# Optimization experiments

Hardware: AMD Instinct MI355X
Metric: run time of the kernel (lower is better)

The kernel has to match this reference:

```python
import jax, jax.numpy as jnp
import numpy as np

B, S, D, H = 2, 2048, 1024, 16
DK = D // H
FF_HIDDEN = 2048  # FeedForward default hidden_dim (fixed, not 4*D)


def setup_inputs() -> dict:
    key = jax.random.key(0)
    ks = jax.random.split(key, 16)
    s = 0.02
    inp = {
        "query": jax.random.normal(ks[0], (B, S, D), jnp.float32),
        "key": jax.random.normal(ks[1], (B, S, D), jnp.float32),
        "value": jax.random.normal(ks[2], (B, S, D), jnp.float32),
        "Wq": jax.random.normal(ks[3], (D, D), jnp.float32) * s,
        "bq": jnp.zeros((D,), jnp.float32),
        "Wk": jax.random.normal(ks[4], (D, D), jnp.float32) * s,
        "bk": jnp.zeros((D,), jnp.float32),
        "Wv": jax.random.normal(ks[5], (D, D), jnp.float32) * s,
        "bv": jnp.zeros((D,), jnp.float32),
        "ln_g": jnp.ones((D,), jnp.float32),
        "ln_b": jnp.zeros((D,), jnp.float32),
        "W1": jax.random.normal(ks[6], (D, FF_HIDDEN), jnp.float32) * s,
        "b1": jnp.zeros((FF_HIDDEN,), jnp.float32),
        "W2": jax.random.normal(ks[7], (FF_HIDDEN, D), jnp.float32) * s,
        "b2": jnp.zeros((D,), jnp.float32),
    }
    return inp


def reference(query, key, value, Wq, bq, Wk, bk, Wv, bv, ln_g, ln_b, W1, b1, W2, b2):
    # QKV projections
    q = query @ Wq + bq  # [B,S,D]
    k = key @ Wk + bk
    v = value @ Wv + bv
    # split heads -> [B,H,S,DK]
    q = q.reshape(B, S, H, DK).transpose(0, 2, 1, 3)
    k = k.reshape(B, S, H, DK).transpose(0, 2, 1, 3)
    v = v.reshape(B, S, H, DK).transpose(0, 2, 1, 3)
    # naive attention: full [B,H,S,S] scores (faithful to source)
    scores = jnp.einsum("bhqd,bhkd->bhqk", q, k) / jnp.sqrt(jnp.float32(DK))
    probs = jax.nn.softmax(scores, axis=-1)  # dropout = identity (eval)
    attn = jnp.einsum("bhqk,bhkd->bhqd", probs, v)
    attn = attn.transpose(0, 2, 1, 3).reshape(B, S, D)
    # LayerNorm
    mu = attn.mean(axis=-1, keepdims=True)
    var = attn.var(axis=-1, keepdims=True)
    ffi = (attn - mu) / jnp.sqrt(var + 1e-5) * ln_g + ln_b
    # FeedForward (dropout = identity in eval)
    h = jax.nn.relu(ffi @ W1 + b1)
    ff = h @ W2 + b2
    return ffi + ff
```

## Files before the change

kernel.cpp:

```cpp
#include <hip/hip_runtime.h>
#include <hip/hip_bf16.h>


#define S_LEN 2048
#define DMODEL 1024
#define NROWS 4096
#define QSCALE (0.125f * 1.4426950408889634f)

typedef __attribute__((ext_vector_type(8))) short short8_t;
typedef __attribute__((ext_vector_type(4))) float f32x4;

__device__ __forceinline__ unsigned short f2bf(float f){
  union { float f; unsigned int u; } a; a.f = f;
  unsigned int r = a.u + 0x7fffu + ((a.u >> 16) & 1u);
  return (unsigned short)(r >> 16);
}
__device__ __forceinline__ unsigned int pack2(float lo, float hi){
  return (unsigned int)f2bf(lo) | ((unsigned int)f2bf(hi) << 16);
}
__device__ __forceinline__ unsigned int cvtpk(float lo, float hi){
  unsigned int r;
  asm("v_cvt_pk_bf16_f32 %0, %1, %2" : "=v"(r) : "v"(lo), "v"(hi));
  return r;
}
__device__ __forceinline__ void gload_lds16(const void* g, void* l){
  __builtin_amdgcn_global_load_lds((const __attribute__((address_space(1))) unsigned int*)g,
                                   (__attribute__((address_space(3))) unsigned int*)l, 16, 0, 0);
}

__global__ __launch_bounds__(256) void cast3_kernel(const float* __restrict__ q,
    const float* __restrict__ k, const float* __restrict__ v, unsigned short* __restrict__ out){
  const float* src = blockIdx.y == 0 ? q : (blockIdx.y == 1 ? k : v);
  size_t i = (size_t)(blockIdx.x * 256 + threadIdx.x) * 8;
  float4 a = *(const float4*)(src + i);
  float4 b = *(const float4*)(src + i + 4);
  uint4 u; u.x = pack2(a.x,a.y); u.y = pack2(a.z,a.w); u.z = pack2(b.x,b.y); u.w = pack2(b.z,b.w);
  *(uint4*)(out + (size_t)blockIdx.y*4194304 + i) = u;
}

__device__ __forceinline__ void tc_body(const float* __restrict__ in,
    unsigned short* __restrict__ out, int R, int C, int bx, int by){
  __shared__ __align__(16) unsigned short tile[64*76];
  int c0 = bx * 64, r0 = by * 64;
  int t = threadIdx.x;
#pragma unroll
  for (int i = 0; i < 4; i++){
    int slot = i*256 + t;
    int r = slot >> 4, c4 = slot & 15;
    float4 v = *(const float4*)(in + (size_t)(r0 + r)*C + c0 + c4*4);
    ushort4 u; u.x = f2bf(v.x); u.y = f2bf(v.y); u.z = f2bf(v.z); u.w = f2bf(v.w);
    *(ushort4*)&tile[r*76 + c4*4] = u;
  }
  __syncthreads();
#pragma unroll
  for (int i = 0; i < 4; i++){
    int slot = i*256 + t;
    int oc = slot >> 4, seg = slot & 15;
    ushort4 u;
    u.x = tile[(seg*4+0)*76 + oc];
    u.y = tile[(seg*4+1)*76 + oc];
    u.z = tile[(seg*4+2)*76 + oc];
    u.w = tile[(seg*4+3)*76 + oc];
    *(ushort4*)(out + (size_t)(c0 + oc)*R + r0 + seg*4) = u;
  }
}
__global__ __launch_bounds__(256) void transpose_cast_f32(const float* __restrict__ in,
    unsigned short* __restrict__ out, int R, int C){
  tc_body(in, out, R, C, blockIdx.x, blockIdx.y);
}
__global__ __launch_bounds__(256) void transpose_cast_w3(const float* __restrict__ w0,
    const float* __restrict__ w1, const float* __restrict__ w2, unsigned short* __restrict__ out){
  const float* in = blockIdx.z == 0 ? w0 : (blockIdx.z == 1 ? w1 : w2);
  tc_body(in, out + (size_t)blockIdx.z*1048576, 1024, 1024, blockIdx.x, blockIdx.y);
}

__global__ __launch_bounds__(256) void transpose_bf16(const unsigned short* __restrict__ in,
    unsigned short* __restrict__ out, int R, int C, int inStride){
  __shared__ __align__(16) unsigned short tile[64*76];
  int c0 = blockIdx.x * 64, r0 = blockIdx.y * 64;
  int t = threadIdx.x;
#pragma unroll
  for (int i = 0; i < 2; i++){
    int slot = i*256 + t;
    int r = slot >> 3, c8 = slot & 7;
    uint4 v = *(const uint4*)(in + (size_t)(r0 + r)*inStride + c0 + c8*8);
    uint2 lo; lo.x = v.x; lo.y = v.y;
    uint2 hi; hi.x = v.z; hi.y = v.w;
    *(uint2*)&tile[r*76 + c8*8]     = lo;
    *(uint2*)&tile[r*76 + c8*8 + 4] = hi;
  }
  __syncthreads();
#pragma unroll
  for (int i = 0; i < 4; i++){
    int slot = i*256 + t;
    int oc = slot >> 4, seg = slot & 15;
    ushort4 u;
    u.x = tile[(seg*4+0)*76 + oc];
    u.y = tile[(seg*4+1)*76 + oc];
    u.z = tile[(seg*4+2)*76 + oc];
    u.w = tile[(seg*4+3)*76 + oc];
    *(ushort4*)(out + (size_t)(c0 + oc)*R + r0 + seg*4) = u;
  }
}

__global__ __launch_bounds__(256) void concat_bias(const float* __restrict__ a,
    const float* __restrict__ b, const float* __restrict__ c, float* __restrict__ o){
  int i = blockIdx.x*256 + threadIdx.x;
  o[i] = i < 1024 ? a[i] : (i < 2048 ? b[i-1024] : c[i-2048]);
}

template<bool OBF16, bool RELU, bool RESID, int NF>
__global__ __launch_bounds__(256, 2) void gemm_bt(
    const unsigned short* __restrict__ A, const unsigned short* __restrict__ Bt,
    const float* __restrict__ bias, float scale, int scale_ncols, size_t aSel,
    unsigned short* __restrict__ Ob, float* __restrict__ Of,
    const float* __restrict__ resid, int M, int N, int K)
{
  __shared__ __align__(16) unsigned short As[128*32];
  __shared__ __align__(16) unsigned short Bs[128*32];
  int tid = threadIdx.x; int lane = tid & 63; int wave = tid >> 6;
  int wr = wave >> 1, wc = wave & 1;
  int m0 = blockIdx.y * 128, n0 = blockIdx.x * (32*NF);
  int qr = lane & 15, g = lane >> 4;
  f32x4 acc[4][NF];
#pragma unroll
  for (int i = 0; i < 4; i++)
#pragma unroll
    for (int j = 0; j < NF; j++) acc[i][j] = (f32x4){0.f,0.f,0.f,0.f};

  const unsigned short* Ag = A + (size_t)(n0 >> 10)*aSel + (size_t)(m0 + (tid >> 2))*K + (tid & 3)*8;
  const unsigned short* Bg = Bt + (size_t)(n0 + (tid >> 2))*K + (tid & 3)*8;
  char* Adst = (char*)As + wave*1024;
  char* Bdst = (char*)Bs + wave*1024;

  for (int k0 = 0; k0 < K; k0 += 32){
    gload_lds16(Ag + k0,                  Adst);
    gload_lds16(Ag + (size_t)64*K + k0,   Adst + 4096);
    gload_lds16(Bg + k0,                  Bdst);
    if constexpr (NF == 4)
      gload_lds16(Bg + (size_t)64*K + k0, Bdst + 4096);
    __syncthreads();
    short8_t af[4], bfv[NF];
#pragma unroll
    for (int mi = 0; mi < 4; mi++)  af[mi]  = *(const short8_t*)&As[(wr*64 + mi*16 + qr)*32 + g*8];
#pragma unroll
    for (int ni = 0; ni < NF; ni++) bfv[ni] = *(const short8_t*)&Bs[(wc*16*NF + ni*16 + qr)*32 + g*8];
#pragma unroll
    for (int mi = 0; mi < 4; mi++)
#pragma unroll
      for (int ni = 0; ni < NF; ni++)
        acc[mi][ni] = __builtin_amdgcn_mfma_f32_16x16x32_bf16(af[mi], bfv[ni], acc[mi][ni], 0, 0, 0);
    __syncthreads();
  }
#pragma unroll
  for (int ni = 0; ni < NF; ni++){
    int col = n0 + wc*16*NF + ni*16 + qr;
    float bs = bias[col];
    float sc = (col < scale_ncols) ? scale : 1.f;
#pragma unroll
    for (int mi = 0; mi < 4; mi++){
#pragma unroll
      for (int r = 0; r < 4; r++){
        int row = m0 + wr*64 + mi*16 + g*4 + r;
        float v = (acc[mi][ni][r] + bs) * sc;
        if constexpr (RELU) v = fmaxf(v, 0.f);
        if constexpr (RESID) v += resid[(size_t)row*N + col];
        if constexpr (OBF16) Ob[(size_t)row*N + col] = f2bf(v);
        else                 Of[(size_t)row*N + col] = v;
      }
    }
  }
}

__global__ __launch_bounds__(256, 4) void flash_attn(
    const unsigned short* __restrict__ qkv,
    const unsigned short* __restrict__ vT,
    float* __restrict__ attn)
{
  __shared__ __align__(16) char smem[40960];
  int tid = threadIdx.x, lane = tid & 63, wave = tid >> 6;
  int bid = blockIdx.x;
  int orig = (bid & 7) * 128 + (bid >> 3);
  int bh = orig >> 5, qb = orig & 31;
  int b = bh >> 4, h = bh & 15;
  int q0 = qb * 64 + wave * 16;
  int qr = lane & 15, g = lane >> 4;

  const unsigned short* qptr = qkv + (size_t)(b*S_LEN + q0 + qr)*3072 + h*64 + g*8;
  short8_t qf0 = *(const short8_t*)qptr;
  short8_t qf1 = *(const short8_t*)(qptr + 32);

  const f32x4 z4 = {0.f,0.f,0.f,0.f};
  f32x4 oacc[4];
#pragma unroll
  for (int tv = 0; tv < 4; tv++) oacc[tv] = z4;
  float lsum = 0.f;

  int lrow = lane >> 3, lslot = lane & 7;
  int sw = (lslot ^ lrow) * 8;
  const unsigned short* kg = qkv + 1024 + (size_t)(b*S_LEN + wave*8 + lrow)*3072 + h*64 + sw;
  const unsigned short* vg = vT + (size_t)(h*64 + wave*8 + lrow)*4096 + b*S_LEN + sw;

  int rx = qr & 7;
  int koff0 = qr*128 + ((g ^ rx) * 16);
  int koff1 = koff0 ^ 64;

  char* Pb = smem + 32768 + wave*2048;
  int gh = g >> 1;
  int pw0 = qr*128 + 8*(g & 1);
  int pr0 = qr*128;

  {
    char* kb_ = smem + wave*1024;
    char* vb_ = smem + 16384 + wave*1024;
    gload_lds16(kg,                       kb_);
    gload_lds16(kg + (size_t)32*3072,     kb_ + 4096);
    gload_lds16(vg,                       vb_);
    gload_lds16(vg + (size_t)32*4096,     vb_ + 4096);
  }

  int cur = 0;
  for (int it = 0; it < S_LEN/64; ++it){
    if (it + 1 < S_LEN/64){
      int kv1 = (it + 1) * 64;
      char* kb_ = smem + (cur^1)*8192 + wave*1024;
      char* vb_ = smem + 16384 + (cur^1)*8192 + wave*1024;
      gload_lds16(kg + (size_t)kv1*3072,        kb_);
      gload_lds16(kg + (size_t)(kv1+32)*3072,   kb_ + 4096);
      gload_lds16(vg + kv1,                     vb_);
      gload_lds16(vg + (size_t)32*4096 + kv1,   vb_ + 4096);
      asm volatile("s_waitcnt vmcnt(4)" ::: "memory");
    } else {
      asm volatile("s_waitcnt vmcnt(0)" ::: "memory");
    }
    __builtin_amdgcn_s_barrier();
    asm volatile("" ::: "memory");

    const char* kb = smem + cur*8192;
    const char* vb = smem + 16384 + cur*8192;

    f32x4 st[4];
    __builtin_amdgcn_s_setprio(1);
#pragma unroll
    for (int t = 0; t < 4; t++){
      short8_t kf0 = *(const short8_t*)(kb + koff0 + t*2048);
      short8_t kf1 = *(const short8_t*)(kb + koff1 + t*2048);
      st[t] = __builtin_amdgcn_mfma_f32_16x16x32_bf16(kf0, qf0, z4, 0, 0, 0);
      st[t] = __builtin_amdgcn_mfma_f32_16x16x32_bf16(kf1, qf1, st[t], 0, 0, 0);
    }
    __builtin_amdgcn_s_setprio(0);

    float ps0 = 0.f, ps1 = 0.f;
#pragma unroll
    for (int t = 0; t < 4; t++){
      float p0 = exp2f(st[t][0]);
      float p1 = exp2f(st[t][1]);
      float p2 = exp2f(st[t][2]);
      float p3 = exp2f(st[t][3]);
      uint2 wv; wv.x = cvtpk(p0, p1); wv.y = cvtpk(p2, p3);
      *(uint2*)(Pb + pw0 + (((2*t + gh) ^ rx) << 4)) = wv;
      ps0 += p0 + p1;
      ps1 += p2 + p3;
    }
    lsum += ps0 + ps1;

    short8_t pf0 = *(const short8_t*)(Pb + pr0 + (((0 + g) ^ rx) << 4));
    short8_t pf1 = *(const short8_t*)(Pb + pr0 + (((4 + g) ^ rx) << 4));

    __builtin_amdgcn_s_setprio(1);
#pragma unroll
    for (int tv = 0; tv < 4; tv++){
      short8_t vf0 = *(const short8_t*)(vb + koff0 + tv*2048);
      short8_t vf1 = *(const short8_t*)(vb + koff1 + tv*2048);
      oacc[tv] = __builtin_amdgcn_mfma_f32_16x16x32_bf16(vf0, pf0, oacc[tv], 0, 0, 0);
      oacc[tv] = __builtin_amdgcn_mfma_f32_16x16x32_bf16(vf1, pf1, oacc[tv], 0, 0, 0);
    }
    __builtin_amdgcn_s_setprio(0);

    asm volatile("s_waitcnt lgkmcnt(0)" ::: "memory");
    __builtin_amdgcn_s_barrier();
    asm volatile("" ::: "memory");
    cur ^= 1;
  }
  lsum += __shfl_xor(lsum, 16, 64);
  lsum += __shfl_xor(lsum, 32, 64);
  float inv = 1.f / lsum;

  __syncthreads();
  float* ot = (float*)(smem + wave*4160);
#pragma unroll
  for (int tv = 0; tv < 4; tv++)
#pragma unroll
    for (int r = 0; r < 4; r++)
      ot[qr*65 + tv*16 + g*4 + r] = oacc[tv][r] * inv;
  __syncthreads();
  int row = lane >> 2, seg = lane & 3;
  const float* src = ot + row*65 + seg*16;
  float* dst = attn + (size_t)(b*S_LEN + qb*64 + wave*16 + row)*DMODEL + h*64 + seg*16;
#pragma unroll
  for (int i = 0; i < 4; i++){
    float4 v; v.x = src[i*4]; v.y = src[i*4+1]; v.z = src[i*4+2]; v.w = src[i*4+3];
    *(float4*)(dst + i*4) = v;
  }
}

__global__ __launch_bounds__(256) void layernorm_kernel(const float* __restrict__ x,
    const float* __restrict__ gw, const float* __restrict__ bw,
    float* __restrict__ y, unsigned short* __restrict__ yb)
{
  int row = blockIdx.x, t = threadIdx.x;
  float4 v = *(const float4*)(x + (size_t)row*DMODEL + t*4);
  float s = (v.x + v.y) + (v.z + v.w);
  float q = (v.x*v.x + v.y*v.y) + (v.z*v.z + v.w*v.w);
#pragma unroll
  for (int off = 1; off < 64; off <<= 1){
    s += __shfl_xor(s, off, 64);
    q += __shfl_xor(q, off, 64);
  }
  __shared__ float red[8];
  if ((t & 63) == 0){ red[(t >> 6)*2] = s; red[(t >> 6)*2 + 1] = q; }
  __syncthreads();
  s = red[0] + red[2] + red[4] + red[6];
  q = red[1] + red[3] + red[5] + red[7];
  float mu = s * (1.f/DMODEL);
  float var = q * (1.f/DMODEL) - mu*mu;
  float rstd = rsqrtf(var + 1e-5f);
  float4 gg = *(const float4*)(gw + t*4);
  float4 bb = *(const float4*)(bw + t*4);
  float4 o;
  o.x = (v.x - mu)*rstd*gg.x + bb.x;
  o.y = (v.y - mu)*rstd*gg.y + bb.y;
  o.z = (v.z - mu)*rstd*gg.z + bb.z;
  o.w = (v.w - mu)*rstd*gg.w + bb.w;
  *(float4*)(y + (size_t)row*DMODEL + t*4) = o;
  uint2 u; u.x = pack2(o.x, o.y); u.y = pack2(o.z, o.w);
  *(uint2*)(yb + (size_t)row*DMODEL + t*4) = u;
}

extern "C" void kernel_launch(void* const* d_in, const int* in_sizes, int n_in,
                              void* d_out, int out_size, void* d_ws, size_t ws_size,
                              hipStream_t stream)
{
  const float* query = (const float*)d_in[0];
  const float* key_  = (const float*)d_in[1];
  const float* value = (const float*)d_in[2];
  const float* Wq = (const float*)d_in[3];
  const float* bq = (const float*)d_in[4];
  const float* Wk = (const float*)d_in[5];
  const float* bk = (const float*)d_in[6];
  const float* Wv = (const float*)d_in[7];
  const float* bv = (const float*)d_in[8];
  const float* ln_g = (const float*)d_in[9];
  const float* ln_b = (const float*)d_in[10];
  const float* W1 = (const float*)d_in[11];
  const float* b1 = (const float*)d_in[12];
  const float* W2 = (const float*)d_in[13];
  const float* b2 = (const float*)d_in[14];

  char* ws = (char*)d_ws;
  unsigned short* qx     = (unsigned short*)(ws + 0);
  unsigned short* WqkvT  = (unsigned short*)(ws + 25165824);
  unsigned short* W1T    = (unsigned short*)(ws + 31457280);
  unsigned short* W2T    = (unsigned short*)(ws + 35651584);
  unsigned short* qkvbuf = (unsigned short*)(ws + 39845888);
  unsigned short* vTb    = (unsigned short*)(ws + 65011712);
  float*          attnf  = (float*)(ws + 73400320);
  unsigned short* hbuf   = (unsigned short*)(ws + 73400320);
  float*          biascat= (float*)(ws + 73400320 + 8388608);
  float*          ffif   = (float*)(ws + 90177536);
  unsigned short* ffib   = (unsigned short*)(ws + 106954752);

  cast3_kernel<<<dim3(2048,3), 256, 0, stream>>>(query, key_, value, qx);
  transpose_cast_w3<<<dim3(16,16,3), 256, 0, stream>>>(Wq, Wk, Wv, WqkvT);
  transpose_cast_f32<<<dim3(32,16), 256, 0, stream>>>(W1, W1T, 1024, 2048);
  transpose_cast_f32<<<dim3(16,32), 256, 0, stream>>>(W2, W2T, 2048, 1024);
  concat_bias<<<12, 256, 0, stream>>>(bq, bk, bv, biascat);

  gemm_bt<true,false,false,4><<<dim3(24,32), 256, 0, stream>>>(
      qx, WqkvT, biascat, QSCALE, 1024, (size_t)4194304, qkvbuf, nullptr, nullptr, 4096, 3072, 1024);
  transpose_bf16<<<dim3(16,64), 256, 0, stream>>>(qkvbuf + 2048, vTb, 4096, 1024, 3072);
  flash_attn<<<1024, 256, 0, stream>>>(qkvbuf, vTb, attnf);
  layernorm_kernel<<<4096, 256, 0, stream>>>(attnf, ln_g, ln_b, ffif, ffib);
  gemm_bt<true,true,false,4><<<dim3(16,32), 256, 0, stream>>>(
      ffib, W1T, b1, 1.f, 0, (size_t)0, hbuf, nullptr, nullptr, 4096, 2048, 1024);
  gemm_bt<false,false,true,2><<<dim3(16,32), 256, 0, stream>>>(
      hbuf, W2T, b2, 1.f, 0, (size_t)0, nullptr, (float*)d_out, ffif, 4096, 1024, 2048);
}
```

Measured before the change: 206.5 us.

## Double-buffer GEMM LDS tiles with K=64 steps and XOR-swizzled layout

Rewrites the bf16 GEMM main loop to double-buffer the A and B shared-memory tiles and prefetch the next K-chunk while computing the current one. It uses manual vmcnt waits and raw barriers in place of __syncthreads. The K step doubles to 64, halving the number of barriers per tile, and an XOR swizzle on the LDS column index is meant to avoid bank conflicts. The cost is double the LDS footprint, which may reduce occupancy, plus hand-counted waitcnt values that must match the number of issued loads.

```diff
diff --git a/kernel.cpp b/kernel.cpp
--- a/kernel.cpp
+++ b/kernel.cpp
@@ -116,9 +116,11 @@
     unsigned short* __restrict__ Ob, float* __restrict__ Of,
     const float* __restrict__ resid, int M, int N, int K)
 {
-  __shared__ __align__(16) unsigned short As[128*32];
-  __shared__ __align__(16) unsigned short Bs[128*32];
-  int tid = threadIdx.x; int lane = tid & 63; int wave = tid >> 6;
+  __shared__ __align__(16) unsigned short As[2*128*64];
+  __shared__ __align__(16) unsigned short Bs[2*32*NF*64];
+  char* AsB = (char*)As;
+  char* BsB = (char*)Bs;
+  int tid = threadIdx.x, lane = tid & 63, wave = tid >> 6;
   int wr = wave >> 1, wc = wave & 1;
   int m0 = blockIdx.y * 128, n0 = blockIdx.x * (32*NF);
   int qr = lane & 15, g = lane >> 4;
@@ -128,29 +130,67 @@
 #pragma unroll
     for (int j = 0; j < NF; j++) acc[i][j] = (f32x4){0.f,0.f,0.f,0.f};
 
-  const unsigned short* Ag = A + (size_t)(n0 >> 10)*aSel + (size_t)(m0 + (tid >> 2))*K + (tid & 3)*8;
-  const unsigned short* Bg = Bt + (size_t)(n0 + (tid >> 2))*K + (tid & 3)*8;
-  char* Adst = (char*)As + wave*1024;
-  char* Bdst = (char*)Bs + wave*1024;
-
-  for (int k0 = 0; k0 < K; k0 += 32){
-    gload_lds16(Ag + k0,                  Adst);
-    gload_lds16(Ag + (size_t)64*K + k0,   Adst + 4096);
-    gload_lds16(Bg + k0,                  Bdst);
-    if constexpr (NF == 4)
-      gload_lds16(Bg + (size_t)64*K + k0, Bdst + 4096);
-    __syncthreads();
-    short8_t af[4], bfv[NF];
-#pragma unroll
-    for (int mi = 0; mi < 4; mi++)  af[mi]  = *(const short8_t*)&As[(wr*64 + mi*16 + qr)*32 + g*8];
-#pragma unroll
-    for (int ni = 0; ni < NF; ni++) bfv[ni] = *(const short8_t*)&Bs[(wc*16*NF + ni*16 + qr)*32 + g*8];
-#pragma unroll
-    for (int mi = 0; mi < 4; mi++)
-#pragma unroll
-      for (int ni = 0; ni < NF; ni++)
-        acc[mi][ni] = __builtin_amdgcn_mfma_f32_16x16x32_bf16(af[mi], bfv[ni], acc[mi][ni], 0, 0, 0);
-    __syncthreads();
+  int lr = lane >> 3, ls = lane & 7;
+  int scol = (ls ^ lr) * 8;
+  const unsigned short* Ag = A + (size_t)(n0 >> 10)*aSel + (size_t)(m0 + wave*32 + lr)*K + scol;
+  const unsigned short* Bg = Bt + (size_t)(n0 + wave*8*NF + lr)*K + scol;
+
+  int rx = qr & 7;
+  int aoff = (wr*64 + qr)*128 + ((g ^ rx) << 4);
+  int boff = (wc*16*NF + qr)*128 + ((g ^ rx) << 4);
+
+  int NT = K >> 6;
+#pragma unroll
+  for (int i = 0; i < 4; i++)
+    gload_lds16(Ag + (size_t)i*8*K, AsB + wave*4096 + i*1024);
+#pragma unroll
+  for (int i = 0; i < NF; i++)
+    gload_lds16(Bg + (size_t)i*8*K, BsB + wave*NF*1024 + i*1024);
+
+  for (int it = 0; it < NT; ++it){
+    int cur = it & 1;
+    if (it + 1 < NT){
+      int k1 = (it + 1) << 6;
+      char* ad = AsB + (cur^1)*16384 + wave*4096;
+      char* bd = BsB + (cur^1)*NF*4096 + wave*NF*1024;
+#pragma unroll
+      for (int i = 0; i < 4; i++)
+        gload_lds16(Ag + (size_t)i*8*K + k1, ad + i*1024);
+#pragma unroll
+      for (int i = 0; i < NF; i++)
+        gload_lds16(Bg + (size_t)i*8*K + k1, bd + i*1024);
+      if constexpr (NF == 4) asm volatile("s_waitcnt vmcnt(8)" ::: "memory");
+      else                   asm volatile("s_waitcnt vmcnt(6)" ::: "memory");
+    } else {
+      asm volatile("s_waitcnt vmcnt(0)" ::: "memory");
+    }
+    __builtin_amdgcn_s_barrier();
+    asm volatile("" ::: "memory");
+
+    const char* ka = AsB + cur*16384;
+    const char* kb = BsB + cur*NF*4096;
+    short8_t af[2][4], bfv[2][NF];
+#pragma unroll
+    for (int mi = 0; mi < 4; mi++){
+      af[0][mi] = *(const short8_t*)(ka + aoff + mi*2048);
+      af[1][mi] = *(const short8_t*)(ka + (aoff^64) + mi*2048);
+    }
+#pragma unroll
+    for (int ni = 0; ni < NF; ni++){
+      bfv[0][ni] = *(const short8_t*)(kb + boff + ni*2048);
+      bfv[1][ni] = *(const short8_t*)(kb + (boff^64) + ni*2048);
+    }
+#pragma unroll
+    for (int kh = 0; kh < 2; kh++)
+#pragma unroll
+      for (int mi = 0; mi < 4; mi++)
+#pragma unroll
+        for (int ni = 0; ni < NF; ni++)
+          acc[mi][ni] = __builtin_amdgcn_mfma_f32_16x16x32_bf16(af[kh][mi], bfv[kh][ni], acc[mi][ni], 0, 0, 0);
+
+    asm volatile("s_waitcnt lgkmcnt(0)" ::: "memory");
+    __builtin_amdgcn_s_barrier();
+    asm volatile("" ::: "memory");
   }
 #pragma unroll
   for (int ni = 0; ni < NF; ni++){
```

Result: faster. 199.8 us (-3.2%).
